# Optimization experiments

Measured on AMD Instinct MI355X. Metric: run time of the kernel, lower is better.

## Reference

```python
import jax, jax.numpy as jnp
import numpy as np

B, S, H = 2, 2048, 2048
NH, KVH, HD = 16, 4, 128
THETA = 10000.0


def setup_inputs() -> dict:
    key = jax.random.key(0)
    k1, k2, k3, k4, k5 = jax.random.split(key, 5)
    scale = 1.0 / np.sqrt(H)
    return {
        "hidden_states": jax.random.normal(k1, (B, S, H), dtype=jnp.float32),
        "Wq": jax.random.normal(k2, (H, NH * HD), dtype=jnp.float32) * scale,
        "Wk": jax.random.normal(k3, (H, KVH * HD), dtype=jnp.float32) * scale,
        "Wv": jax.random.normal(k4, (H, KVH * HD), dtype=jnp.float32) * scale,
        "Wo": jax.random.normal(k5, (NH * HD, H), dtype=jnp.float32) * scale,
    }


def _rotate_half(x):
    x1, x2 = x[..., : HD // 2], x[..., HD // 2 :]
    return jnp.concatenate((-x2, x1), axis=-1)


def _rope_cos_sin(seq_len):
    # inv_freq: [HD/2]
    inv_freq = 1.0 / (THETA ** (jnp.arange(0, HD, 2, dtype=jnp.float32) / HD))
    pos = jnp.arange(seq_len, dtype=jnp.float32)
    freqs = pos[:, None] * inv_freq[None, :]          # [S, HD/2]
    emb = jnp.concatenate((freqs, freqs), axis=-1)    # [S, HD]
    return jnp.cos(emb), jnp.sin(emb)


def reference(hidden_states, Wq, Wk, Wv, Wo):
    b, s, _ = hidden_states.shape
    n_rep = NH // KVH

    # projections -> [B, S, heads, HD]
    q = (hidden_states @ Wq).reshape(b, s, NH, HD)
    k = (hidden_states @ Wk).reshape(b, s, KVH, HD)
    v = (hidden_states @ Wv).reshape(b, s, KVH, HD)

    # RoPE (cos/sin broadcast over head dim, matching cos.unsqueeze(-2))
    cos, sin = _rope_cos_sin(s)
    cos = cos[None, :, None, :]  # [1, S, 1, HD]
    sin = sin[None, :, None, :]
    q = q * cos + _rotate_half(q) * sin
    k = k * cos + _rotate_half(k) * sin

    # repeat_kv: [B, S, KVH, HD] -> [B, S, NH, HD]
    k = jnp.repeat(k, n_rep, axis=2)
    v = jnp.repeat(v, n_rep, axis=2)

    # causal SDPA
    scores = jnp.einsum("bqhd,bkhd->bhqk", q, k) / jnp.sqrt(jnp.float32(HD))
    causal = jnp.tril(jnp.ones((s, s), dtype=bool))
    scores = jnp.where(causal[None, None], scores, jnp.finfo(scores.dtype).min)
    probs = jax.nn.softmax(scores, axis=-1)
    ctx = jnp.einsum("bhqk,bkhd->bqhd", probs, v)     # [B, S, NH, HD]

    out = ctx.reshape(b, s, NH * HD) @ Wo             # [B, S, H]
    return out
```

## Files before the change

kernel.cpp:

```cpp
#include <hip/hip_runtime.h>
#include <stdint.h>
#include <math.h>

#define BB 2
#define SS 2048
#define HH 2048
#define NH 16
#define KVH 4
#define HD 128
#define BSZ (BB*SS)
#define QW (NH*HD)
#define KVW (KVH*HD)

typedef __attribute__((ext_vector_type(8))) short s16x8;
typedef __attribute__((ext_vector_type(4))) float f32x4;

typedef const unsigned int __attribute__((address_space(1)))* gas_ptr;
typedef unsigned int __attribute__((address_space(3)))* las_ptr;

__device__ __forceinline__ unsigned short f2b(float x) {
    unsigned u = __builtin_bit_cast(unsigned, x);
    unsigned r = u + 0x7fffu + ((u >> 16) & 1u);
    return (unsigned short)(r >> 16);
}
__device__ __forceinline__ float b2f(unsigned short h) {
    unsigned u = ((unsigned)h) << 16;
    return __builtin_bit_cast(float, u);
}

__device__ __forceinline__ void gload_lds16(const void* g, void* l) {
    __builtin_amdgcn_global_load_lds((gas_ptr)g, (las_ptr)l, 16, 0, 0);
}

template<int FN>
__device__ __forceinline__ void stage_tile_dp(
    const unsigned short* __restrict__ A,
    const unsigned short* __restrict__ Bt,
    int m0, int c0, int kt, unsigned short* lds)
{
    constexpr int TILEA = 256 * 32;
    constexpr int TILEB = FN * 64 * 32;
    constexpr int TILE  = TILEA + TILEB;
    unsigned short* buf = lds + (size_t)(kt & 3) * TILE;
    const int tid = threadIdx.x;
    const int wub = (tid >> 6) * 64;
    const int k0 = kt * 32;
#pragma unroll
    for (int q = 0; q < 2; ++q) {
        int blk = q * 512 + tid;
        int row = blk >> 2, pb = blk & 3, lb = pb ^ (row & 3);
        gload_lds16(A + (size_t)(m0 + row) * HH + k0 + lb * 8,
                    buf + (size_t)(q * 512 + wub) * 8);
    }
    unsigned short* bbuf = buf + TILEA;
#pragma unroll
    for (int q = 0; q < FN / 2; ++q) {
        int blk = q * 512 + tid;
        int row = blk >> 2, pb = blk & 3, lb = pb ^ (row & 3);
        gload_lds16(Bt + (size_t)(c0 + row) * HH + k0 + lb * 8,
                    bbuf + (size_t)(q * 512 + wub) * 8);
    }
}

template<int FN>
__device__ __forceinline__ void compute_tile_dp(
    int t, unsigned short* lds, f32x4 acc[8][4])
{
    constexpr int TILEA = 256 * 32;
    constexpr int TILEB = FN * 64 * 32;
    constexpr int TILE  = TILEA + TILEB;
    unsigned short* buf  = lds + (size_t)(t & 3) * TILE;
    unsigned short* bbuf = buf + TILEA;
    const int tid = threadIdx.x;
    const int lane = tid & 63;
    const int quad = lane >> 4, l15 = lane & 15;
    const int wm = (tid >> 6) >> 2, wn = (tid >> 6) & 3;

    s16x8 bf[FN];
#pragma unroll
    for (int fn = 0; fn < FN; ++fn) {
        int row = wn * (FN * 16) + fn * 16 + l15;
        bf[fn] = *(const s16x8*)(bbuf + row * 32 + ((quad ^ (row & 3)) * 8));
    }
#pragma unroll
    for (int g = 0; g < 2; ++g) {
        s16x8 af[4];
#pragma unroll
        for (int j = 0; j < 4; ++j) {
            int row = wm * 128 + (g * 4 + j) * 16 + l15;
            af[j] = *(const s16x8*)(buf + row * 32 + ((quad ^ (row & 3)) * 8));
        }
        __builtin_amdgcn_s_setprio(1);
#pragma unroll
        for (int j = 0; j < 4; ++j)
#pragma unroll
            for (int fn = 0; fn < FN; ++fn)
                acc[g * 4 + j][fn] = __builtin_amdgcn_mfma_f32_16x16x32_bf16(
                    af[j], bf[fn], acc[g * 4 + j][fn], 0, 0, 0);
        __builtin_amdgcn_s_setprio(0);
    }
}

template<int FN>
__device__ __forceinline__ void gemm_dp(
    const unsigned short* __restrict__ A,
    const unsigned short* __restrict__ Bt,
    int m0, int c0, unsigned short* lds, f32x4 acc[8][4])
{
#pragma unroll
    for (int i = 0; i < 8; ++i)
#pragma unroll
        for (int fn = 0; fn < 4; ++fn) acc[i][fn] = (f32x4){0.f, 0.f, 0.f, 0.f};

    constexpr int NT = HH / 32;
    stage_tile_dp<FN>(A, Bt, m0, c0, 0, lds);
    stage_tile_dp<FN>(A, Bt, m0, c0, 1, lds);
    stage_tile_dp<FN>(A, Bt, m0, c0, 2, lds);

    for (int t = 0; t < NT - 3; ++t) {
        __builtin_amdgcn_s_barrier();
        __builtin_amdgcn_sched_barrier(0);
        stage_tile_dp<FN>(A, Bt, m0, c0, t + 3, lds);
        if constexpr (FN == 4) asm volatile("s_waitcnt vmcnt(12)" ::: "memory");
        else                   asm volatile("s_waitcnt vmcnt(9)"  ::: "memory");
        __builtin_amdgcn_sched_barrier(0);
        __builtin_amdgcn_s_barrier();
        __builtin_amdgcn_sched_barrier(0);
        compute_tile_dp<FN>(t, lds, acc);
    }
    for (int t = NT - 3; t < NT; ++t) {
        __builtin_amdgcn_s_barrier();
        __builtin_amdgcn_sched_barrier(0);
        if constexpr (FN == 4) {
            if (t == NT - 3)      asm volatile("s_waitcnt vmcnt(8)" ::: "memory");
            else if (t == NT - 2) asm volatile("s_waitcnt vmcnt(4)" ::: "memory");
            else                  asm volatile("s_waitcnt vmcnt(0)" ::: "memory");
        } else {
            if (t == NT - 3)      asm volatile("s_waitcnt vmcnt(6)" ::: "memory");
            else if (t == NT - 2) asm volatile("s_waitcnt vmcnt(3)" ::: "memory");
            else                  asm volatile("s_waitcnt vmcnt(0)" ::: "memory");
        }
        __builtin_amdgcn_sched_barrier(0);
        __builtin_amdgcn_s_barrier();
        __builtin_amdgcn_sched_barrier(0);
        compute_tile_dp<FN>(t, lds, acc);
    }
}

__global__ __launch_bounds__(512, 2) void gemm_qkv(
    const unsigned short* __restrict__ Ah,
    const unsigned short* __restrict__ Wqt,
    const unsigned short* __restrict__ Wkt,
    const unsigned short* __restrict__ Wvt,
    unsigned short* __restrict__ Qb,
    unsigned short* __restrict__ Kb,
    unsigned short* __restrict__ Vb)
{
    __shared__ __align__(16) unsigned short lds[4 * (256 * 32 + 256 * 32)];
    const int id  = blockIdx.y * 12 + blockIdx.x;
    const int swz = (id & 7) * 24 + (id >> 3);
    const int nblk = (swz % 12) * 256;
    const int m0   = (swz / 12) * 256;
    const unsigned short* Bt;
    unsigned short* C;
    int c0, ldc;
    if (nblk < QW)            { Bt = Wqt; C = Qb; c0 = nblk;            ldc = QW;  }
    else if (nblk < QW + KVW) { Bt = Wkt; C = Kb; c0 = nblk - QW;       ldc = KVW; }
    else                      { Bt = Wvt; C = Vb; c0 = nblk - QW - KVW; ldc = KVW; }

    f32x4 acc[8][4];
    gemm_dp<4>(Ah, Bt, m0, c0, lds, acc);

    const int tid = threadIdx.x;
    const int lane = tid & 63;
    const int quad = lane >> 4, l15 = lane & 15;
    const int wm = (tid >> 6) >> 2, wn = (tid >> 6) & 3;
#pragma unroll
    for (int fr = 0; fr < 8; ++fr)
#pragma unroll
        for (int fn = 0; fn < 4; ++fn)
#pragma unroll
            for (int r = 0; r < 4; ++r) {
                int row = m0 + wm * 128 + fr * 16 + quad * 4 + r;
                int col = c0 + wn * 64 + fn * 16 + l15;
                C[(size_t)row * ldc + col] = f2b(acc[fr][fn][r]);
            }
}

__global__ __launch_bounds__(512, 2) void gemm_out(
    const unsigned short* __restrict__ ctx,
    const unsigned short* __restrict__ Wot,
    float* __restrict__ out)
{
    __shared__ __align__(16) unsigned short lds[4 * (256 * 32 + 128 * 32)];
    const int id  = blockIdx.y * 16 + blockIdx.x;
    const int swz = (id & 7) * 32 + (id >> 3);
    const int c0 = (swz & 15) * 128;
    const int m0 = (swz >> 4) * 256;

    f32x4 acc[8][4];
    gemm_dp<2>(ctx, Wot, m0, c0, lds, acc);

    const int tid = threadIdx.x;
    const int lane = tid & 63;
    const int quad = lane >> 4, l15 = lane & 15;
    const int wm = (tid >> 6) >> 2, wn = (tid >> 6) & 3;
#pragma unroll
    for (int fr = 0; fr < 8; ++fr)
#pragma unroll
        for (int fn = 0; fn < 2; ++fn)
#pragma unroll
            for (int r = 0; r < 4; ++r) {
                int row = m0 + wm * 128 + fr * 16 + quad * 4 + r;
                int col = c0 + wn * 32 + fn * 16 + l15;
                out[(size_t)row * HH + col] = acc[fr][fn][r];
            }
}

__global__ __launch_bounds__(256) void prep(
    const float* __restrict__ hidden, unsigned short* __restrict__ Ah,
    const float* __restrict__ Wq, const float* __restrict__ Wk,
    const float* __restrict__ Wv, const float* __restrict__ Wo,
    unsigned short* __restrict__ Wqt, unsigned short* __restrict__ Wkt,
    unsigned short* __restrict__ Wvt, unsigned short* __restrict__ Wot)
{
    __shared__ float t[32][33];
    const int bx = blockIdx.x;
    if (bx < 8192) {
        int i = (bx * 256 + threadIdx.x) * 4;
        float4 v = *(const float4*)(hidden + i);
        ushort4 o = make_ushort4(f2b(v.x), f2b(v.y), f2b(v.z), f2b(v.w));
        *(ushort4*)(Ah + i) = o;
        return;
    }
    const int b2 = bx - 8192;
    const int z  = b2 >> 12;
    const int xy = b2 & 4095;
    const float* in;
    unsigned short* out;
    int N;
    if (z == 0)      { in = Wq; out = Wqt; N = QW;  }
    else if (z == 1) { in = Wk; out = Wkt; N = KVW; }
    else if (z == 2) { in = Wv; out = Wvt; N = KVW; }
    else             { in = Wo; out = Wot; N = HH;  }
    const int n0 = (xy & 63) * 32;
    if (n0 >= N) return;
    const int k0 = (xy >> 6) * 32;

    const int c = threadIdx.x & 31, r = threadIdx.x >> 5;
#pragma unroll
    for (int j = 0; j < 4; ++j)
        t[r + j * 8][c] = in[(size_t)(k0 + r + j * 8) * N + n0 + c];
    __syncthreads();
#pragma unroll
    for (int j = 0; j < 4; ++j)
        out[(size_t)(n0 + r + j * 8) * HH + k0 + c] = f2b(t[c][r + j * 8]);
}

__global__ __launch_bounds__(256) void vtrans_bf16(const unsigned short* __restrict__ Vb,
                                                   unsigned short* __restrict__ Vtg)
{
    __shared__ unsigned short t[32][33];
    const int s0 = blockIdx.x * 32, c0 = blockIdx.y * 32, b = blockIdx.z;
    const int cc = threadIdx.x & 31, r = threadIdx.x >> 5;
#pragma unroll
    for (int j = 0; j < 4; ++j)
        t[r + j * 8][cc] = Vb[(size_t)(b * SS + s0 + r + j * 8) * KVW + c0 + cc];
    __syncthreads();
#pragma unroll
    for (int j = 0; j < 4; ++j)
        Vtg[(size_t)(b * KVW + c0 + r + j * 8) * SS + s0 + cc] = t[cc][r + j * 8];
}

__global__ __launch_bounds__(256) void rope_all(unsigned short* __restrict__ Qb,
                                                unsigned short* __restrict__ Kb)
{
    int idx = blockIdx.x * 256 + threadIdx.x;
    const int totalQ = BSZ * NH * 8;
    unsigned short* X;
    int nheads; float mul;
    if (idx < totalQ) { X = Qb; nheads = NH; mul = 0.08838834764831845f; }
    else              { X = Kb; nheads = KVH; mul = 1.0f; idx -= totalQ; }
    const int j0 = (idx & 7) * 8;
    const int t  = idx >> 3;
    const int hh = t % nheads;
    const int bs = t / nheads;
    const float s = (float)(bs & (SS - 1));
    size_t base = (size_t)bs * ((size_t)nheads * HD) + (size_t)hh * HD + j0;
    s16x8 v1 = *(const s16x8*)(X + base);
    s16x8 v2 = *(const s16x8*)(X + base + 64);
    s16x8 o1, o2;
#pragma unroll
    for (int e = 0; e < 8; ++e) {
        float inv = exp2f(-0.2076205063f * (float)(j0 + e));
        float ang = s * inv;
        float c = __cosf(ang), sn = __sinf(ang);
        float x1 = b2f((unsigned short)v1[e]);
        float x2 = b2f((unsigned short)v2[e]);
        o1[e] = (short)f2b((x1 * c - x2 * sn) * mul);
        o2[e] = (short)f2b((x2 * c + x1 * sn) * mul);
    }
    *(s16x8*)(X + base)      = o1;
    *(s16x8*)(X + base + 64) = o2;
}

__global__ __launch_bounds__(256) void attn_mfma(
    const unsigned short* __restrict__ Qb,
    const unsigned short* __restrict__ Kb,
    const unsigned short* __restrict__ Vtg,
    unsigned short* __restrict__ ctx)
{
    const int b   = blockIdx.x;
    const int h   = blockIdx.y;
    const int qtp = 31 - blockIdx.z;
    const int kvh = h >> 2;
    const int q0  = qtp * 64;
    const int tid = threadIdx.x;
    const int lane = tid & 63, wave = tid >> 6;
    const int quad = lane >> 4, l15 = lane & 15;
    const int lo8 = l15 & 7, hi8 = l15 >> 3;

    __shared__ __align__(16) unsigned short Ks[64 * 128];
    __shared__ __align__(16) unsigned short Vt[128 * 64];
    __shared__ __align__(16) unsigned short Ps[4][16 * 64];

    const int krb = tid >> 4;
    const int c8k = tid & 15;
    const int dv  = tid >> 3;
    const int c8v = tid & 7;

    const unsigned short* Kbase = Kb  + (size_t)b * SS * KVW + kvh * HD;
    const unsigned short* Vbase = Vtg + (size_t)(b * KVW + kvh * HD) * SS;

    s16x8 qf[4];
    {
        const unsigned short* qrow =
            Qb + (size_t)(b * SS + q0 + wave * 16 + l15) * QW + h * HD;
#pragma unroll
        for (int dc = 0; dc < 4; ++dc)
            qf[dc] = *(const s16x8*)(qrow + dc * 32 + quad * 8);
    }

    f32x4 oacc[8];
#pragma unroll
    for (int i = 0; i < 8; ++i) oacc[i] = (f32x4){0.f, 0.f, 0.f, 0.f};
    f32x4 lacc = (f32x4){0.f, 0.f, 0.f, 0.f};

    const s16x8 vone = {0x3F80, 0x3F80, 0x3F80, 0x3F80,
                        0x3F80, 0x3F80, 0x3F80, 0x3F80};

    s16x8 kpre[4], vpre[4];
#pragma unroll
    for (int u = 0; u < 4; ++u) {
        kpre[u] = *(const s16x8*)(Kbase + (size_t)(u * 16 + krb) * KVW + c8k * 8);
        vpre[u] = *(const s16x8*)(Vbase + (size_t)(u * 32 + dv) * SS + c8v * 8);
    }

    const int nkt = qtp + 1;
    for (int kt = 0; kt < nkt; ++kt) {
        const int k0 = kt * 64;
        __syncthreads();

#pragma unroll
        for (int u = 0; u < 4; ++u) {
            *(s16x8*)(Ks + (u * 16 + krb) * 128 + ((c8k ^ krb) * 8)) = kpre[u];
            *(s16x8*)(Vt + (u * 32 + dv) * 64 + ((c8v ^ (dv & 7)) * 8)) = vpre[u];
        }
        __syncthreads();

        if (kt + 1 < nkt) {
            const int kn = k0 + 64;
#pragma unroll
            for (int u = 0; u < 4; ++u) {
                kpre[u] = *(const s16x8*)(Kbase + (size_t)(kn + u * 16 + krb) * KVW + c8k * 8);
                vpre[u] = *(const s16x8*)(Vbase + (size_t)(u * 32 + dv) * SS + kn + c8v * 8);
            }
        }

        f32x4 sc[4];
#pragma unroll
        for (int tk = 0; tk < 4; ++tk) sc[tk] = (f32x4){0.f, 0.f, 0.f, 0.f};
        __builtin_amdgcn_s_setprio(1);
#pragma unroll
        for (int tk = 0; tk < 4; ++tk) {
#pragma unroll
            for (int dc = 0; dc < 4; ++dc) {
                s16x8 kf = *(const s16x8*)(Ks + (tk * 16 + l15) * 128
                                              + (((dc * 4 + quad) ^ l15) * 8));
                sc[tk] = __builtin_amdgcn_mfma_f32_16x16x32_bf16(qf[dc], kf, sc[tk], 0, 0, 0);
            }
        }
        __builtin_amdgcn_s_setprio(0);

        unsigned short* pw = &Ps[wave][0];
        const bool lastt = (kt == nkt - 1);
#pragma unroll
        for (int tk = 0; tk < 4; ++tk) {
            float p[4];
#pragma unroll
            for (int r = 0; r < 4; ++r)
                p[r] = __expf(sc[tk][r] - 10.0f);
            if (lastt) {
                const int colr = tk * 16 + l15 - wave * 16 - quad * 4;
#pragma unroll
                for (int r = 0; r < 4; ++r)
                    if (colr > r) p[r] = 0.f;
            }
            const int cb = tk * 2 + hi8;
            const int row0 = quad * 4;
#pragma unroll
            for (int r = 0; r < 4; ++r)
                pw[(row0 + r) * 64 + (((cb ^ ((row0 + r) & 7)) << 3) | lo8)] = f2b(p[r]);
        }

        s16x8 pf[2];
#pragma unroll
        for (int kc = 0; kc < 2; ++kc)
            pf[kc] = *(const s16x8*)(pw + l15 * 64 + (((kc * 4 + quad) ^ lo8) << 3));
        __builtin_amdgcn_s_setprio(1);
        lacc = __builtin_amdgcn_mfma_f32_16x16x32_bf16(pf[0], vone, lacc, 0, 0, 0);
        lacc = __builtin_amdgcn_mfma_f32_16x16x32_bf16(pf[1], vone, lacc, 0, 0, 0);
#pragma unroll
        for (int dt = 0; dt < 8; ++dt) {
#pragma unroll
            for (int kc = 0; kc < 2; ++kc) {
                s16x8 vf = *(const s16x8*)(Vt + (dt * 16 + l15) * 64
                                              + (((kc * 4 + quad) ^ lo8) * 8));
                oacc[dt] = __builtin_amdgcn_mfma_f32_16x16x32_bf16(pf[kc], vf, oacc[dt], 0, 0, 0);
            }
        }
        __builtin_amdgcn_s_setprio(0);
    }

    float linv[4];
#pragma unroll
    for (int r = 0; r < 4; ++r) linv[r] = 1.0f / lacc[r];
#pragma unroll
    for (int dt = 0; dt < 8; ++dt)
#pragma unroll
        for (int r = 0; r < 4; ++r) {
            int row = b * SS + q0 + wave * 16 + quad * 4 + r;
            ctx[(size_t)row * QW + h * HD + dt * 16 + l15] =
                f2b(oacc[dt][r] * linv[r]);
        }
}

extern "C" void kernel_launch(void* const* d_in, const int* in_sizes, int n_in,
                              void* d_out, int out_size, void* d_ws, size_t ws_size,
                              hipStream_t stream)
{
    const float* hidden = (const float*)d_in[0];
    const float* Wq = (const float*)d_in[1];
    const float* Wk = (const float*)d_in[2];
    const float* Wv = (const float*)d_in[3];
    const float* Wo = (const float*)d_in[4];
    float* out = (float*)d_out;

    unsigned short* Ah  = (unsigned short*)d_ws;
    unsigned short* Wqt = Ah  + (size_t)BSZ * HH;
    unsigned short* Wkt = Wqt + (size_t)QW * HH;
    unsigned short* Wvt = Wkt + (size_t)KVW * HH;
    unsigned short* Wot = Wvt + (size_t)KVW * HH;
    unsigned short* Qb  = Wot + (size_t)HH * QW;
    unsigned short* Kb  = Qb  + (size_t)BSZ * QW;
    unsigned short* Vb  = Kb  + (size_t)BSZ * KVW;
    unsigned short* ctx = Vb  + (size_t)BSZ * KVW;
    unsigned short* Vtg = ctx + (size_t)BSZ * QW;

    prep<<<24576, 256, 0, stream>>>(hidden, Ah, Wq, Wk, Wv, Wo,
                                    Wqt, Wkt, Wvt, Wot);

    gemm_qkv<<<dim3(12, 16), 512, 0, stream>>>(Ah, Wqt, Wkt, Wvt, Qb, Kb, Vb);

    vtrans_bf16<<<dim3(SS / 32, KVW / 32, BB), 256, 0, stream>>>(Vb, Vtg);

    rope_all<<<(BSZ * (NH + KVH) * 8) / 256, 256, 0, stream>>>(Qb, Kb);

    attn_mfma<<<dim3(BB, NH, SS / 64), 256, 0, stream>>>(Qb, Kb, Vtg, ctx);

    gemm_out<<<dim3(16, 16), 512, 0, stream>>>(ctx, Wot, out);
}
```

Baseline: 294.5 us.

## Restructure projection GEMMs into 8-phase double-buffered pipeline with 64-wide K tiles

Replaces the 4-stage, 32-wide K-tile GEMM main loop used by the QKV and output projections with a 2-buffer, 64-wide K-tile schedule. Each K step is split into four phases that interleave half-tile global-to-LDS loads with MFMA groups, separated by barriers and an 8-way XOR swizzle. The aim is finer overlap of loads with matrix math and fewer barrier rounds per K element. In exchange it adds many more barriers per iteration and has a shallower prefetch depth, which may expose memory latency.

```diff
diff --git a/kernel.cpp b/kernel.cpp
--- a/kernel.cpp
+++ b/kernel.cpp
@@ -33,117 +33,164 @@
 }
 
 template<int FN>
-__device__ __forceinline__ void stage_tile_dp(
+__device__ __forceinline__ void stage_half(
+    const unsigned short* __restrict__ src, int rowbase, int k0,
+    unsigned short* dst)
+{
+    const int tid = threadIdx.x;
+#pragma unroll
+    for (int q = 0; q < 2; ++q) {
+        int row = (tid >> 3) + q * 64;
+        int sl  = (tid & 7) ^ (row & 7);
+        gload_lds16(src + (size_t)(rowbase + row) * HH + k0 + sl * 8,
+                    dst + (q * 512 + tid) * 8);
+    }
+}
+
+__device__ __forceinline__ s16x8 ldsr(const unsigned short* base,
+                                      int r, int kh, int quad)
+{
+    return *(const s16x8*)(base + r * 64 + (((kh * 4 + quad) ^ (r & 7)) * 8));
+}
+
+#define SBAR() do { __builtin_amdgcn_sched_barrier(0); \
+                    __builtin_amdgcn_s_barrier();       \
+                    __builtin_amdgcn_sched_barrier(0); } while (0)
+
+template<int FN>
+__device__ __forceinline__ void gemm8p(
     const unsigned short* __restrict__ A,
     const unsigned short* __restrict__ Bt,
-    int m0, int c0, int kt, unsigned short* lds)
-{
-    constexpr int TILEA = 256 * 32;
-    constexpr int TILEB = FN * 64 * 32;
-    constexpr int TILE  = TILEA + TILEB;
-    unsigned short* buf = lds + (size_t)(kt & 3) * TILE;
-    const int tid = threadIdx.x;
-    const int wub = (tid >> 6) * 64;
-    const int k0 = kt * 32;
-#pragma unroll
-    for (int q = 0; q < 2; ++q) {
-        int blk = q * 512 + tid;
-        int row = blk >> 2, pb = blk & 3, lb = pb ^ (row & 3);
-        gload_lds16(A + (size_t)(m0 + row) * HH + k0 + lb * 8,
-                    buf + (size_t)(q * 512 + wub) * 8);
-    }
-    unsigned short* bbuf = buf + TILEA;
-#pragma unroll
-    for (int q = 0; q < FN / 2; ++q) {
-        int blk = q * 512 + tid;
-        int row = blk >> 2, pb = blk & 3, lb = pb ^ (row & 3);
-        gload_lds16(Bt + (size_t)(c0 + row) * HH + k0 + lb * 8,
-                    bbuf + (size_t)(q * 512 + wub) * 8);
-    }
-}
-
-template<int FN>
-__device__ __forceinline__ void compute_tile_dp(
-    int t, unsigned short* lds, f32x4 acc[8][4])
-{
-    constexpr int TILEA = 256 * 32;
-    constexpr int TILEB = FN * 64 * 32;
-    constexpr int TILE  = TILEA + TILEB;
-    unsigned short* buf  = lds + (size_t)(t & 3) * TILE;
-    unsigned short* bbuf = buf + TILEA;
-    const int tid = threadIdx.x;
-    const int lane = tid & 63;
+    int m0, int c0, unsigned short* lds, f32x4 acc[8][FN])
+{
+    constexpr int NT    = HH / 64;
+    constexpr int BUFE  = (2 + FN / 2) * 8192;
+    constexpr int ABOFF = (FN / 2) * 8192;
+    const int tid  = threadIdx.x;
+    const int lane = tid & 63, wave = tid >> 6;
     const int quad = lane >> 4, l15 = lane & 15;
-    const int wm = (tid >> 6) >> 2, wn = (tid >> 6) & 3;
-
-    s16x8 bf[FN];
-#pragma unroll
-    for (int fn = 0; fn < FN; ++fn) {
-        int row = wn * (FN * 16) + fn * 16 + l15;
-        bf[fn] = *(const s16x8*)(bbuf + row * 32 + ((quad ^ (row & 3)) * 8));
-    }
-#pragma unroll
-    for (int g = 0; g < 2; ++g) {
-        s16x8 af[4];
-#pragma unroll
-        for (int j = 0; j < 4; ++j) {
-            int row = wm * 128 + (g * 4 + j) * 16 + l15;
-            af[j] = *(const s16x8*)(buf + row * 32 + ((quad ^ (row & 3)) * 8));
-        }
+    const int wm = wave >> 2, wn = wave & 3;
+    const int arow0 = wm * 128 + l15;
+    const int brow0 = wn * (FN * 16) + l15;
+
+#pragma unroll
+    for (int i = 0; i < 8; ++i)
+#pragma unroll
+        for (int fc = 0; fc < FN; ++fc) acc[i][fc] = (f32x4){0.f, 0.f, 0.f, 0.f};
+
+    unsigned short* buf0 = lds;
+    unsigned short* buf1 = lds + BUFE;
+
+    stage_half<FN>(Bt, c0, 0, buf0);
+    if constexpr (FN == 4) stage_half<FN>(Bt, c0 + 128, 0, buf0 + 8192);
+    stage_half<FN>(A, m0, 0, buf0 + ABOFF);
+    stage_half<FN>(A, m0 + 128, 0, buf0 + ABOFF + 8192);
+    stage_half<FN>(Bt, c0, 64, buf1);
+    if constexpr (FN == 4) {
+        stage_half<FN>(Bt, c0 + 128, 64, buf1 + 8192);
+        asm volatile("s_waitcnt vmcnt(4)" ::: "memory");
+    } else {
+        asm volatile("s_waitcnt vmcnt(2)" ::: "memory");
+    }
+    SBAR();
+
+#pragma unroll 2
+    for (int T = 0; T < NT; ++T) {
+        unsigned short* buf = (T & 1) ? buf1 : buf0;
+        unsigned short* nbuf = (T & 1) ? buf0 : buf1;
+        const unsigned short* Bb = buf;
+        const unsigned short* Ab = buf + ABOFF;
+        const int k1 = (T + 1) * 64, k2 = (T + 2) * 64;
+
+        s16x8 b[FN][2], a01[2][2];
+#pragma unroll
+        for (int fc = 0; fc < FN; ++fc)
+#pragma unroll
+            for (int kh = 0; kh < 2; ++kh)
+                b[fc][kh] = ldsr(Bb, brow0 + fc * 16, kh, quad);
+#pragma unroll
+        for (int fr = 0; fr < 2; ++fr)
+#pragma unroll
+            for (int kh = 0; kh < 2; ++kh)
+                a01[fr][kh] = ldsr(Ab, arow0 + fr * 16, kh, quad);
+        if (T + 1 < NT) stage_half<FN>(A, m0, k1, nbuf + ABOFF);
+        SBAR();
         __builtin_amdgcn_s_setprio(1);
 #pragma unroll
-        for (int j = 0; j < 4; ++j)
-#pragma unroll
-            for (int fn = 0; fn < FN; ++fn)
-                acc[g * 4 + j][fn] = __builtin_amdgcn_mfma_f32_16x16x32_bf16(
-                    af[j], bf[fn], acc[g * 4 + j][fn], 0, 0, 0);
+        for (int fr = 0; fr < 2; ++fr)
+#pragma unroll
+            for (int fc = 0; fc < FN; ++fc)
+#pragma unroll
+                for (int kh = 0; kh < 2; ++kh)
+                    acc[fr][fc] = __builtin_amdgcn_mfma_f32_16x16x32_bf16(
+                        a01[fr][kh], b[fc][kh], acc[fr][fc], 0, 0, 0);
         __builtin_amdgcn_s_setprio(0);
-    }
-}
-
-template<int FN>
-__device__ __forceinline__ void gemm_dp(
-    const unsigned short* __restrict__ A,
-    const unsigned short* __restrict__ Bt,
-    int m0, int c0, unsigned short* lds, f32x4 acc[8][4])
-{
-#pragma unroll
-    for (int i = 0; i < 8; ++i)
-#pragma unroll
-        for (int fn = 0; fn < 4; ++fn) acc[i][fn] = (f32x4){0.f, 0.f, 0.f, 0.f};
-
-    constexpr int NT = HH / 32;
-    stage_tile_dp<FN>(A, Bt, m0, c0, 0, lds);
-    stage_tile_dp<FN>(A, Bt, m0, c0, 1, lds);
-    stage_tile_dp<FN>(A, Bt, m0, c0, 2, lds);
-
-    for (int t = 0; t < NT - 3; ++t) {
-        __builtin_amdgcn_s_barrier();
+        SBAR();
+
+        s16x8 a23[2][2], a45[2][2];
+#pragma unroll
+        for (int fr = 0; fr < 2; ++fr)
+#pragma unroll
+            for (int kh = 0; kh < 2; ++kh) {
+                a23[fr][kh] = ldsr(Ab, arow0 + (2 + fr) * 16, kh, quad);
+                a45[fr][kh] = ldsr(Ab, arow0 + (4 + fr) * 16, kh, quad);
+            }
+        if (T + 1 < NT) stage_half<FN>(A, m0 + 128, k1, nbuf + ABOFF + 8192);
+        SBAR();
+        __builtin_amdgcn_s_setprio(1);
+#pragma unroll
+        for (int fr = 0; fr < 2; ++fr)
+#pragma unroll
+            for (int fc = 0; fc < FN; ++fc)
+#pragma unroll
+                for (int kh = 0; kh < 2; ++kh)
+                    acc[2 + fr][fc] = __builtin_amdgcn_mfma_f32_16x16x32_bf16(
+                        a23[fr][kh], b[fc][kh], acc[2 + fr][fc], 0, 0, 0);
+        __builtin_amdgcn_s_setprio(0);
+        SBAR();
+
+        s16x8 a67[2][2];
+#pragma unroll
+        for (int fr = 0; fr < 2; ++fr)
+#pragma unroll
+            for (int kh = 0; kh < 2; ++kh)
+                a67[fr][kh] = ldsr(Ab, arow0 + (6 + fr) * 16, kh, quad);
+        if (T + 2 < NT) stage_half<FN>(Bt, c0, k2, buf);
+        SBAR();
+        __builtin_amdgcn_s_setprio(1);
+#pragma unroll
+        for (int fr = 0; fr < 2; ++fr)
+#pragma unroll
+            for (int fc = 0; fc < FN; ++fc)
+#pragma unroll
+                for (int kh = 0; kh < 2; ++kh)
+                    acc[4 + fr][fc] = __builtin_amdgcn_mfma_f32_16x16x32_bf16(
+                        a45[fr][kh], b[fc][kh], acc[4 + fr][fc], 0, 0, 0);
+        __builtin_amdgcn_s_setprio(0);
+        SBAR();
+
+        if constexpr (FN == 4) {
+            if (T + 2 < NT) stage_half<FN>(Bt, c0 + 128, k2, buf + 8192);
+        }
         __builtin_amdgcn_sched_barrier(0);
-        stage_tile_dp<FN>(A, Bt, m0, c0, t + 3, lds);
-        if constexpr (FN == 4) asm volatile("s_waitcnt vmcnt(12)" ::: "memory");
-        else                   asm volatile("s_waitcnt vmcnt(9)"  ::: "memory");
-        __builtin_amdgcn_sched_barrier(0);
-        __builtin_amdgcn_s_barrier();
-        __builtin_amdgcn_sched_barrier(0);
-        compute_tile_dp<FN>(t, lds, acc);
-    }
-    for (int t = NT - 3; t < NT; ++t) {
-        __builtin_amdgcn_s_barrier();
-        __builtin_amdgcn_sched_barrier(0);
-        if constexpr (FN == 4) {
-            if (t == NT - 3)      asm volatile("s_waitcnt vmcnt(8)" ::: "memory");
-            else if (t == NT - 2) asm volatile("s_waitcnt vmcnt(4)" ::: "memory");
-            else                  asm volatile("s_waitcnt vmcnt(0)" ::: "memory");
-        } else {
-            if (t == NT - 3)      asm volatile("s_waitcnt vmcnt(6)" ::: "memory");
-            else if (t == NT - 2) asm volatile("s_waitcnt vmcnt(3)" ::: "memory");
-            else                  asm volatile("s_waitcnt vmcnt(0)" ::: "memory");
-        }
-        __builtin_amdgcn_sched_barrier(0);
-        __builtin_amdgcn_s_barrier();
-        __builtin_amdgcn_sched_barrier(0);
-        compute_tile_dp<FN>(t, lds, acc);
+        if (T <= NT - 3) {
+            if constexpr (FN == 4) asm volatile("s_waitcnt vmcnt(4)" ::: "memory");
+            else                   asm volatile("s_waitcnt vmcnt(2)" ::: "memory");
+        } else if (T == NT - 2) {
+            asm volatile("s_waitcnt vmcnt(0)" ::: "memory");
+        }
+        SBAR();
+        __builtin_amdgcn_s_setprio(1);
+#pragma unroll
+        for (int fr = 0; fr < 2; ++fr)
+#pragma unroll
+            for (int fc = 0; fc < FN; ++fc)
+#pragma unroll
+                for (int kh = 0; kh < 2; ++kh)
+                    acc[6 + fr][fc] = __builtin_amdgcn_mfma_f32_16x16x32_bf16(
+                        a67[fr][kh], b[fc][kh], acc[6 + fr][fc], 0, 0, 0);
+        __builtin_amdgcn_s_setprio(0);
+        SBAR();
     }
 }
 
@@ -156,7 +203,7 @@
     unsigned short* __restrict__ Kb,
     unsigned short* __restrict__ Vb)
 {
-    __shared__ __align__(16) unsigned short lds[4 * (256 * 32 + 256 * 32)];
+    __shared__ __align__(16) unsigned short lds[2 * 4 * 8192];
     const int id  = blockIdx.y * 12 + blockIdx.x;
     const int swz = (id & 7) * 24 + (id >> 3);
     const int nblk = (swz % 12) * 256;
@@ -169,7 +216,7 @@
     else                      { Bt = Wvt; C = Vb; c0 = nblk - QW - KVW; ldc = KVW; }
 
     f32x4 acc[8][4];
-    gemm_dp<4>(Ah, Bt, m0, c0, lds, acc);
+    gemm8p<4>(Ah, Bt, m0, c0, lds, acc);
 
     const int tid = threadIdx.x;
     const int lane = tid & 63;
@@ -178,12 +225,12 @@
 #pragma unroll
     for (int fr = 0; fr < 8; ++fr)
 #pragma unroll
-        for (int fn = 0; fn < 4; ++fn)
+        for (int fc = 0; fc < 4; ++fc)
 #pragma unroll
             for (int r = 0; r < 4; ++r) {
                 int row = m0 + wm * 128 + fr * 16 + quad * 4 + r;
-                int col = c0 + wn * 64 + fn * 16 + l15;
-                C[(size_t)row * ldc + col] = f2b(acc[fr][fn][r]);
+                int col = c0 + wn * 64 + fc * 16 + l15;
+                C[(size_t)row * ldc + col] = f2b(acc[fr][fc][r]);
             }
 }
 
@@ -192,14 +239,14 @@
     const unsigned short* __restrict__ Wot,
     float* __restrict__ out)
 {
-    __shared__ __align__(16) unsigned short lds[4 * (256 * 32 + 128 * 32)];
+    __shared__ __align__(16) unsigned short lds[2 * 3 * 8192];
     const int id  = blockIdx.y * 16 + blockIdx.x;
     const int swz = (id & 7) * 32 + (id >> 3);
     const int c0 = (swz & 15) * 128;
     const int m0 = (swz >> 4) * 256;
 
-    f32x4 acc[8][4];
-    gemm_dp<2>(ctx, Wot, m0, c0, lds, acc);
+    f32x4 acc[8][2];
+    gemm8p<2>(ctx, Wot, m0, c0, lds, acc);
 
     const int tid = threadIdx.x;
     const int lane = tid & 63;
@@ -208,12 +255,12 @@
 #pragma unroll
     for (int fr = 0; fr < 8; ++fr)
 #pragma unroll
-        for (int fn = 0; fn < 2; ++fn)
+        for (int fc = 0; fc < 2; ++fc)
 #pragma unroll
             for (int r = 0; r < 4; ++r) {
                 int row = m0 + wm * 128 + fr * 16 + quad * 4 + r;
-                int col = c0 + wn * 32 + fn * 16 + l15;
-                out[(size_t)row * HH + col] = acc[fr][fn][r];
+                int col = c0 + wn * 32 + fc * 16 + l15;
+                out[(size_t)row * HH + col] = acc[fr][fc][r];
             }
 }
 
```

Result: faster. 273.3 us (-7.2%).
